# Performance work log

Measured on AMD Instinct MI355X. Metric: run time of the kernel, lower is better.

The kernel has to match this reference:

```python
import jax, jax.numpy as jnp
import numpy as np

B, NQ, NKV, D = 2, 2048, 4096, 1024
H, DH = 16, 64            # qk_channels = v_channels = 1024 -> 16 heads x 64
HID = 2 * int(4.0 * D)    # GEGLU produces 8192 -> split into 2x4096
EPS = 1e-6


def layernorm(x, scale, bias):
    mu = jnp.mean(x, axis=-1, keepdims=True)
    var = jnp.mean(jnp.square(x - mu), axis=-1, keepdims=True)
    return (x - mu) * jax.lax.rsqrt(var + EPS) * scale + bias


def setup_inputs() -> dict:
    key = jax.random.key(0)
    ks = jax.random.split(key, 12)
    s = 0.02
    return {
        "inputs_q": jax.random.normal(ks[0], (B, NQ, D), jnp.float32),
        "inputs_kv": jax.random.normal(ks[1], (B, NKV, D), jnp.float32),
        "ln_q_scale": jnp.ones((D,), jnp.float32),
        "ln_q_bias": jnp.zeros((D,), jnp.float32),
        "ln_kv_scale": jnp.ones((D,), jnp.float32),
        "ln_kv_bias": jnp.zeros((D,), jnp.float32),
        "Wq": s * jax.random.normal(ks[2], (D, H, DH), jnp.float32),
        "bq": jnp.zeros((H, DH), jnp.float32),
        "Wk": s * jax.random.normal(ks[3], (D, H, DH), jnp.float32),
        "bk": jnp.zeros((H, DH), jnp.float32),
        "Wv": s * jax.random.normal(ks[4], (D, H, DH), jnp.float32),
        "bv": jnp.zeros((H, DH), jnp.float32),
        "Wo": s * jax.random.normal(ks[5], (H, DH, D), jnp.float32),
        "bo": jnp.zeros((D,), jnp.float32),
        "ln2_scale": jnp.ones((D,), jnp.float32),
        "ln2_bias": jnp.zeros((D,), jnp.float32),
        "W1": s * jax.random.normal(ks[6], (D, HID), jnp.float32),
        "b1": jnp.zeros((HID,), jnp.float32),
        "W2": s * jax.random.normal(ks[7], (HID // 2, D), jnp.float32),
        "b2": jnp.zeros((D,), jnp.float32),
    }


def reference(inputs_q, inputs_kv, ln_q_scale, ln_q_bias, ln_kv_scale, ln_kv_bias,
              Wq, bq, Wk, bk, Wv, bv, Wo, bo, ln2_scale, ln2_bias, W1, b1, W2, b2):
    ln_q = layernorm(inputs_q, ln_q_scale, ln_q_bias)
    ln_kv = layernorm(inputs_kv, ln_kv_scale, ln_kv_bias)
    # multi-head projections: DenseGeneral to (H, DH)
    q = jnp.einsum('bqd,dhe->bqhe', ln_q, Wq) + bq
    k = jnp.einsum('bkd,dhe->bkhe', ln_kv, Wk) + bk
    v = jnp.einsum('bkd,dhe->bkhe', ln_kv, Wv) + bv
    # scaled dot-product attention (full score matrix, as in source)
    attn = jnp.einsum('bqhd,bkhd->bhqk', q, k) / np.sqrt(DH).astype(np.float32)
    attn = jax.nn.softmax(attn, axis=-1)
    o = jnp.einsum('bhqk,bkhd->bqhd', attn, v)
    # output projection contracting (H, DH)
    x = jnp.einsum('bqhd,hdo->bqo', o, Wo) + bo
    x = x + inputs_q  # query residual
    # GEGLU MLP
    h = layernorm(x, ln2_scale, ln2_bias)
    h = jnp.dot(h, W1) + b1
    a, g = jnp.split(h, 2, axis=-1)
    h = a * jax.nn.gelu(g)  # approximate (tanh) gelu, flax default
    y = jnp.dot(h, W2) + b2
    return x + y
```

## Files before the change

### kernel.cpp

```cpp
#include <hip/hip_runtime.h>

typedef unsigned short u16;
typedef unsigned int u32;
typedef float f32x4 __attribute__((ext_vector_type(4)));
typedef float f32x16 __attribute__((ext_vector_type(16)));
typedef __bf16 bf16x8 __attribute__((ext_vector_type(8)));
typedef short s16x8 __attribute__((ext_vector_type(8)));
typedef short s16x4 __attribute__((ext_vector_type(4)));
typedef u32 u32x4 __attribute__((ext_vector_type(4)));

#define MFMA16(a, b, c) __builtin_amdgcn_mfma_f32_16x16x32_bf16((a), (b), (c), 0, 0, 0)
#define MFMA32(a, b, c) __builtin_amdgcn_mfma_f32_32x32x16_bf16((a), (b), (c), 0, 0, 0)

typedef const __attribute__((address_space(1))) void* gas1_t;
typedef __attribute__((address_space(3))) void* las3_t;
#define GLDS16(g, l) __builtin_amdgcn_global_load_lds((gas1_t)(g), (las3_t)(l), 16, 0, 0)

static __device__ __forceinline__ u16 f2bf(float f) {
  u32 u = __builtin_bit_cast(u32, f);
  u += 0x7FFFu + ((u >> 16) & 1u);
  return (u16)(u >> 16);
}
static __device__ __forceinline__ u32 cvtpk(float lo, float hi) {
  u32 r;
  asm("v_cvt_pk_bf16_f32 %0, %1, %2" : "=v"(r) : "v"(lo), "v"(hi));
  return r;
}
static __device__ __forceinline__ float gelu_t(float g) {
  float u = 0.7978845608f * (g + 0.044715f * g * g * g);
  float e = __expf(2.0f * u);
  float t = 1.0f - 2.0f / (e + 1.0f);
  return 0.5f * g * (1.0f + t);
}

__global__ __launch_bounds__(256) void prep_weights(const float* __restrict__ Wq,
                                                    const float* __restrict__ Wk,
                                                    const float* __restrict__ Wv,
                                                    const float* __restrict__ Wo,
                                                    const float* __restrict__ W1,
                                                    const float* __restrict__ W2,
                                                    u16* __restrict__ wqt,
                                                    u16* __restrict__ wkvt,
                                                    u16* __restrict__ wot,
                                                    u16* __restrict__ w1i,
                                                    u16* __restrict__ w2t, float qsc) {
  __shared__ u16 t[64][72];
  const int id = blockIdx.x;
  const int tid = threadIdx.x;
  auto tileT = [&](const float* in, u16* out, int K, int N, int k0, int n0, float scale) {
#pragma unroll
    for (int i = 0; i < 16; ++i) {
      int idx = tid + i * 256;
      int r = idx >> 6, c = idx & 63;
      t[r][c] = f2bf(in[(size_t)(k0 + r) * N + n0 + c] * scale);
    }
    __syncthreads();
#pragma unroll
    for (int i = 0; i < 16; ++i) {
      int idx = tid + i * 256;
      int r = idx >> 6, c = idx & 63;
      out[(size_t)(n0 + r) * K + k0 + c] = t[c][r];
    }
  };
  if (id < 256) {
    tileT(Wq, wqt, 1024, 1024, (id & 15) * 64, (id >> 4) * 64, qsc);
  } else if (id < 512) {
    int i2 = id - 256;
    tileT(Wk, wkvt, 1024, 1024, (i2 & 15) * 64, (i2 >> 4) * 64, 1.0f);
  } else if (id < 768) {
    int i2 = id - 512;
    tileT(Wv, wkvt + 1024 * 1024, 1024, 1024, (i2 & 15) * 64, (i2 >> 4) * 64, 1.0f);
  } else if (id < 1024) {
    int i2 = id - 768;
    tileT(Wo, wot, 1024, 1024, (i2 & 15) * 64, (i2 >> 4) * 64, 1.0f);
  } else if (id < 3072) {
    int i2 = id - 1024;
    int k0 = (i2 & 15) * 64, n0 = (i2 >> 4) * 64;
#pragma unroll
    for (int i = 0; i < 16; ++i) {
      int idx = tid + i * 256;
      int r = idx >> 6, c = idx & 63;
      int np = n0 + c;
      int orig = ((np >> 5) << 4) + (np & 15) + (((np >> 4) & 1) << 12);
      t[r][c] = f2bf(W1[(size_t)(k0 + r) * 8192 + orig]);
    }
    __syncthreads();
#pragma unroll
    for (int i = 0; i < 16; ++i) {
      int idx = tid + i * 256;
      int r = idx >> 6, c = idx & 63;
      w1i[(size_t)(n0 + r) * 1024 + k0 + c] = t[c][r];
    }
  } else {
    int i3 = id - 3072;
    tileT(W2, w2t, 4096, 1024, (i3 & 63) * 64, (i3 >> 6) * 64, 1.0f);
  }
}

__global__ __launch_bounds__(256) void ln_fused(const float* __restrict__ xq,
                                                const float* __restrict__ xkv,
                                                const float* __restrict__ scq,
                                                const float* __restrict__ biq,
                                                const float* __restrict__ sckv,
                                                const float* __restrict__ bikv,
                                                u16* __restrict__ outq,
                                                u16* __restrict__ outkv) {
  const int id = blockIdx.x;
  const bool isq = id < 4096;
  const int row = isq ? id : id - 4096;
  const float* x = isq ? xq : xkv;
  const float* sc = isq ? scq : sckv;
  const float* bi = isq ? biq : bikv;
  u16* out = isq ? outq : outkv;
  int tid = threadIdx.x;
  float4 v = ((const float4*)(x + (size_t)row * 1024))[tid];
  float s = v.x + v.y + v.z + v.w;
  float s2 = v.x * v.x + v.y * v.y + v.z * v.z + v.w * v.w;
  for (int m = 1; m < 64; m <<= 1) {
    s += __shfl_xor(s, m);
    s2 += __shfl_xor(s2, m);
  }
  __shared__ float rs[4], rs2[4];
  int wave = tid >> 6, lane = tid & 63;
  if (lane == 0) { rs[wave] = s; rs2[wave] = s2; }
  __syncthreads();
  s = rs[0] + rs[1] + rs[2] + rs[3];
  s2 = rs2[0] + rs2[1] + rs2[2] + rs2[3];
  float mu = s * (1.0f / 1024.0f);
  float var = s2 * (1.0f / 1024.0f) - mu * mu;
  float inv = rsqrtf(var + 1e-6f);
  float4 scv = ((const float4*)sc)[tid];
  float4 biv = ((const float4*)bi)[tid];
  s16x4 o;
  o[0] = (short)f2bf((v.x - mu) * inv * scv.x + biv.x);
  o[1] = (short)f2bf((v.y - mu) * inv * scv.y + biv.y);
  o[2] = (short)f2bf((v.z - mu) * inv * scv.z + biv.z);
  o[3] = (short)f2bf((v.w - mu) * inv * scv.w + biv.w);
  *(s16x4*)(out + (size_t)row * 1024 + tid * 4) = o;
}

template <int MODE>
__global__ __launch_bounds__(256) void gemm_nt(const u16* __restrict__ A,
                                               const u16* __restrict__ Bt,
                                               const float* __restrict__ bias,
                                               const float* __restrict__ resid,
                                               void* __restrict__ Cout,
                                               int M, int N, int K, float bias_scale) {
  __shared__ u16 As[128 * 64];
  __shared__ u16 Bs[128 * 64];
  const int nbx = gridDim.x;
  const int nwg = nbx * gridDim.y;
  const int wg0 = blockIdx.y * nbx + blockIdx.x;
  const int wg = (nwg & 7) ? wg0 : (wg0 & 7) * (nwg >> 3) + (wg0 >> 3);
  const int m0 = (wg % nbx) * 128, n0 = (wg / nbx) * 128;
  const int tid = threadIdx.x;
  const int lane = tid & 63, wave = tid >> 6;
  const int wm = (wave >> 1) * 64, wn = (wave & 1) * 64;
  const int lr = lane & 15, hi4 = lane >> 4;
  f32x4 acc[4][4] = {};
  for (int k0 = 0; k0 < K; k0 += 64) {
#pragma unroll
    for (int i = 0; i < 4; ++i) {
      int s = i * 256 + tid;
      int r = s >> 3, slot = s & 7;
      int gslot = slot ^ (r & 7);
      int ldst = (i * 256 + wave * 64) * 8;
      GLDS16(A + (size_t)(m0 + r) * K + k0 + gslot * 8, &As[ldst]);
      GLDS16(Bt + (size_t)(n0 + r) * K + k0 + gslot * 8, &Bs[ldst]);
    }
    __syncthreads();
#pragma unroll
    for (int ks = 0; ks < 2; ++ks) {
      const int sl = ((ks * 4 + hi4) ^ (lr & 7)) * 8;
      bf16x8 af[4], bfr[4];
#pragma unroll
      for (int t = 0; t < 4; ++t) {
        af[t] = __builtin_bit_cast(bf16x8, *(const s16x8*)&As[(wm + t * 16 + lr) * 64 + sl]);
        bfr[t] = __builtin_bit_cast(bf16x8, *(const s16x8*)&Bs[(wn + t * 16 + lr) * 64 + sl]);
      }
#pragma unroll
      for (int mt = 0; mt < 4; ++mt)
#pragma unroll
        for (int nt = 0; nt < 4; ++nt)
          acc[mt][nt] = MFMA16(af[mt], bfr[nt], acc[mt][nt]);
    }
    __syncthreads();
  }
#pragma unroll
  for (int mt = 0; mt < 4; ++mt) {
#pragma unroll
    for (int nt = 0; nt < 4; ++nt) {
      const int ncol = n0 + wn + nt * 16 + lr;
      const float bv = bias[ncol] * bias_scale;
      const int mbase = m0 + wm + mt * 16 + hi4 * 4;
#pragma unroll
      for (int r = 0; r < 4; ++r) {
        const int m = mbase + r;
        const float val = acc[mt][nt][r] + bv;
        if constexpr (MODE == 0) {
          ((u16*)Cout)[(size_t)m * N + ncol] = f2bf(val);
        } else {
          ((float*)Cout)[(size_t)m * N + ncol] = val + resid[(size_t)m * N + ncol];
        }
      }
    }
  }
}

template <int MODE>
__global__ __launch_bounds__(512, 2) void gemm256(const u16* __restrict__ A,
                                                  const u16* __restrict__ Bt,
                                                  const float* __restrict__ bias,
                                                  const float* __restrict__ bias2,
                                                  u16* __restrict__ Cout,
                                                  u16* __restrict__ Vout,
                                                  int M, int N, int K, int nmajor) {
  __shared__ __align__(16) u16 sA[2][2][256 * 32];
  __shared__ __align__(16) u16 sB[2][2][256 * 32];
  const int nbx = M >> 8, nby = N >> 8;
  const int nblk = nbx * nby;
  const int cpx = nblk >> 3;
  const int wg0 = blockIdx.x;
  const int wg = (wg0 & 7) * cpx + (wg0 >> 3);
  int mi, ni;
  if (nmajor) { ni = wg % nby; mi = wg / nby; } else { mi = wg % nbx; ni = wg / nbx; }
  const int m0 = mi << 8, n0 = ni << 8;
  const int tid = threadIdx.x;
  const int lane = tid & 63, wave = tid >> 6;
  const int wr = wave >> 2, wc = wave & 3;
  const int lr = lane & 15, hi4 = lane >> 4;
  const int rdoct = (hi4 ^ ((lr >> 1) & 3)) * 8;
  const int NT = K >> 6;

  auto stageA = [&](int t, int kh) {
#pragma unroll
    for (int i = 0; i < 2; ++i) {
      int idx = i * 512 + tid;
      int r = idx >> 2, go = (idx & 3) ^ ((r >> 1) & 3);
      GLDS16(A + (size_t)(m0 + r) * K + t * 64 + kh * 32 + go * 8,
             &sA[t & 1][kh][(i * 512 + wave * 64) * 8]);
    }
  };
  auto stageB = [&](int t, int kh) {
#pragma unroll
    for (int i = 0; i < 2; ++i) {
      int idx = i * 512 + tid;
      int r = idx >> 2, go = (idx & 3) ^ ((r >> 1) & 3);
      GLDS16(Bt + (size_t)(n0 + r) * K + t * 64 + kh * 32 + go * 8,
             &sB[t & 1][kh][(i * 512 + wave * 64) * 8]);
    }
  };

  f32x4 acc[8][4] = {};
  bf16x8 af[4], bf[4];

  stageA(0, 0); stageB(0, 0); stageA(0, 1); stageB(0, 1);
  asm volatile("s_waitcnt vmcnt(4)" ::: "memory");
  __builtin_amdgcn_s_barrier();
  __builtin_amdgcn_sched_barrier(0);

  for (int t = 0; t < NT; ++t) {
    const int buf = t & 1;
    const bool pre = (t + 1 < NT);
#pragma unroll
    for (int kh = 0; kh < 2; ++kh) {
#pragma unroll
      for (int nt = 0; nt < 4; ++nt)
        bf[nt] = __builtin_bit_cast(bf16x8,
            *(const s16x8*)&sB[buf][kh][(wc * 64 + nt * 16 + lr) * 32 + rdoct]);
#pragma unroll
      for (int mf = 0; mf < 4; ++mf)
        af[mf] = __builtin_bit_cast(bf16x8,
            *(const s16x8*)&sA[buf][kh][(wr * 128 + mf * 16 + lr) * 32 + rdoct]);
      if (pre) stageA(t + 1, kh);
      __builtin_amdgcn_s_barrier();
      asm volatile("s_waitcnt lgkmcnt(0)" ::: "memory");
      __builtin_amdgcn_sched_barrier(0);
      __builtin_amdgcn_s_setprio(1);
#pragma unroll
      for (int mf = 0; mf < 4; ++mf)
#pragma unroll
        for (int nt = 0; nt < 4; ++nt)
          acc[mf][nt] = MFMA16(af[mf], bf[nt], acc[mf][nt]);
      __builtin_amdgcn_s_setprio(0);
      __builtin_amdgcn_s_barrier();
      __builtin_amdgcn_sched_barrier(0);
#pragma unroll
      for (int mf = 0; mf < 4; ++mf)
        af[mf] = __builtin_bit_cast(bf16x8,
            *(const s16x8*)&sA[buf][kh][(wr * 128 + (4 + mf) * 16 + lr) * 32 + rdoct]);
      if (pre) stageB(t + 1, kh);
      __builtin_amdgcn_s_barrier();
      asm volatile("s_waitcnt lgkmcnt(0)" ::: "memory");
      __builtin_amdgcn_sched_barrier(0);
      __builtin_amdgcn_s_setprio(1);
#pragma unroll
      for (int mf = 0; mf < 4; ++mf)
#pragma unroll
        for (int nt = 0; nt < 4; ++nt)
          acc[4 + mf][nt] = MFMA16(af[mf], bf[nt], acc[4 + mf][nt]);
      __builtin_amdgcn_s_setprio(0);
      if (pre)
        asm volatile("s_waitcnt vmcnt(4)" ::: "memory");
      else
        asm volatile("s_waitcnt vmcnt(0)" ::: "memory");
      __builtin_amdgcn_s_barrier();
      __builtin_amdgcn_sched_barrier(0);
    }
  }

  if constexpr (MODE == 0) {
#pragma unroll
    for (int mf = 0; mf < 8; ++mf) {
#pragma unroll
      for (int nt = 0; nt < 4; ++nt) {
        const int ncol = n0 + wc * 64 + nt * 16 + lr;
        const int mbase = m0 + wr * 128 + mf * 16 + hi4 * 4;
        const bool isk = ncol < 1024;
        const int vc = isk ? ncol : ncol - 1024;
        const float bv = isk ? bias[ncol] : bias2[vc];
#pragma unroll
        for (int r = 0; r < 4; ++r) {
          const int m = mbase + r;
          const float val = acc[mf][nt][r] + bv;
          if (isk) {
            Cout[(size_t)m * 1024 + ncol] = f2bf(val);
          } else {
            size_t vidx = ((size_t)((m >> 12) * 1024 + vc) << 12) | (size_t)(m & 4095);
            Vout[vidx] = f2bf(val);
          }
        }
      }
    }
  } else {
#pragma unroll
    for (int mf = 0; mf < 8; ++mf) {
      const int mbase = m0 + wr * 128 + mf * 16 + hi4 * 4;
#pragma unroll
      for (int p = 0; p < 2; ++p) {
        const int oc = (((n0 + wc * 64 + p * 32) >> 5) << 4) + lr;
        const float ba = bias[oc];
        const float bg = bias[oc + 4096];
#pragma unroll
        for (int r = 0; r < 4; ++r) {
          const int m = mbase + r;
          float a = acc[mf][2 * p][r] + ba;
          float g = acc[mf][2 * p + 1][r] + bg;
          Cout[(size_t)m * 4096 + oc] = f2bf(a * gelu_t(g));
        }
      }
    }
  }
}

__global__ __launch_bounds__(256, 2) void flash_attn(const u16* __restrict__ Qg,
                                                     const u16* __restrict__ Kg,
                                                     const u16* __restrict__ Vt,
                                                     u16* __restrict__ Og) {
  __shared__ u16 Ks[2][64 * 64];
  __shared__ u16 Vs[2][64 * 64];
  const int id = blockIdx.x;
  const int bh = (id & 7) * 4 + ((id >> 3) & 3);
  const int qb = id >> 5;
  const int b = bh >> 4, h = bh & 15;
  const int q0 = qb * 128;
  const int tid = threadIdx.x;
  const int lane = tid & 63, wave = tid >> 6;
  const int lq = lane & 31, hi = lane >> 5;
  const u16* Kbase = Kg + (size_t)(b * 4096) * 1024 + h * 64;
  const u16* Vbase = Vt + (size_t)((b * 16 + h) * 64) * 4096;
  bf16x8 qf[4];
  const size_t qrow = (size_t)(b * 2048 + q0 + wave * 32 + lq);
#pragma unroll
  for (int dc = 0; dc < 4; ++dc)
    qf[dc] = __builtin_bit_cast(bf16x8, *(const s16x8*)&Qg[qrow * 1024 + h * 64 + dc * 16 + hi * 8]);

  f32x16 oacc0 = {}, oacc1 = {};
  float lrun = 0.0f;

  auto stage = [&](int buf, int tile) {
    const int kv0 = tile * 64;
#pragma unroll
    for (int i = 0; i < 2; ++i) {
      int s = i * 256 + tid;
      int r = s >> 3;
      int inb = ((s & 7) * 16) ^ ((r & 7) << 4);
      GLDS16(Kbase + (size_t)(kv0 + r) * 1024 + (inb >> 1), &Ks[buf][(i * 256 + wave * 64) * 8]);
    }
#pragma unroll
    for (int i = 0; i < 2; ++i) {
      int s = i * 256 + tid;
      int r = s >> 3;
      int inb = ((s & 7) * 16) ^ ((r & 7) << 4);
      GLDS16(Vbase + (size_t)r * 4096 + kv0 + (inb >> 1), &Vs[buf][(i * 256 + wave * 64) * 8]);
    }
  };

  stage(0, 0);
  __syncthreads();
  int cur = 0;
  for (int t = 0; t < 64; ++t) {
    if (t < 63) stage(cur ^ 1, t + 1);
    f32x16 sA = {}, sB = {};
    __builtin_amdgcn_s_setprio(1);
#pragma unroll
    for (int dc = 0; dc < 4; ++dc) {
      int row = lq;
      int inb = (dc * 32 + hi * 16) ^ ((row & 7) << 4);
      bf16x8 kf = __builtin_bit_cast(bf16x8, *(const s16x8*)&Ks[cur][row * 64 + (inb >> 1)]);
      sA = MFMA32(kf, qf[dc], sA);
    }
#pragma unroll
    for (int dc = 0; dc < 4; ++dc) {
      int row = 32 + lq;
      int inb = (dc * 32 + hi * 16) ^ ((row & 7) << 4);
      bf16x8 kf = __builtin_bit_cast(bf16x8, *(const s16x8*)&Ks[cur][row * 64 + (inb >> 1)]);
      sB = MFMA32(kf, qf[dc], sB);
    }
    __builtin_amdgcn_s_setprio(0);
    float ts = 0.0f;
#pragma unroll
    for (int i = 0; i < 16; ++i) {
      float p = __builtin_amdgcn_exp2f(sA[i]);
      sA[i] = p;
      ts += p;
    }
#pragma unroll
    for (int i = 0; i < 16; ++i) {
      float p = __builtin_amdgcn_exp2f(sB[i]);
      sB[i] = p;
      ts += p;
    }
    ts += __shfl_xor(ts, 32);
    lrun += ts;
    u32 wa[8], wb[8];
#pragma unroll
    for (int i = 0; i < 8; ++i) wa[i] = cvtpk(sA[2 * i], sA[2 * i + 1]);
#pragma unroll
    for (int i = 0; i < 8; ++i) wb[i] = cvtpk(sB[2 * i], sB[2 * i + 1]);
    u32 a0 = wa[0], c0 = wa[2];
    asm("v_permlane32_swap_b32 %0, %1" : "+v"(a0), "+v"(c0));
    u32 a1 = wa[1], c1 = wa[3];
    asm("v_permlane32_swap_b32 %0, %1" : "+v"(a1), "+v"(c1));
    u32 a2 = wa[4], c2 = wa[6];
    asm("v_permlane32_swap_b32 %0, %1" : "+v"(a2), "+v"(c2));
    u32 a3 = wa[5], c3 = wa[7];
    asm("v_permlane32_swap_b32 %0, %1" : "+v"(a3), "+v"(c3));
    u32 e0 = wb[0], g0 = wb[2];
    asm("v_permlane32_swap_b32 %0, %1" : "+v"(e0), "+v"(g0));
    u32 e1 = wb[1], g1 = wb[3];
    asm("v_permlane32_swap_b32 %0, %1" : "+v"(e1), "+v"(g1));
    u32 e2 = wb[4], g2 = wb[6];
    asm("v_permlane32_swap_b32 %0, %1" : "+v"(e2), "+v"(g2));
    u32 e3 = wb[5], g3 = wb[7];
    asm("v_permlane32_swap_b32 %0, %1" : "+v"(e3), "+v"(g3));
    u32x4 t00 = {a0, a1, c0, c1};
    u32x4 t01 = {a2, a3, c2, c3};
    u32x4 t10 = {e0, e1, g0, g1};
    u32x4 t11 = {e2, e3, g2, g3};
    bf16x8 p00 = __builtin_bit_cast(bf16x8, t00);
    bf16x8 p01 = __builtin_bit_cast(bf16x8, t01);
    bf16x8 p10 = __builtin_bit_cast(bf16x8, t10);
    bf16x8 p11 = __builtin_bit_cast(bf16x8, t11);
    __builtin_amdgcn_s_setprio(1);
#pragma unroll
    for (int st = 0; st < 2; ++st) {
      bf16x8 pc0 = st ? p10 : p00;
      bf16x8 pc1 = st ? p11 : p01;
#pragma unroll
      for (int c = 0; c < 2; ++c) {
        bf16x8 pf = c ? pc1 : pc0;
        {
          int row = lq;
          int inb = (st * 64 + c * 32 + hi * 16) ^ ((row & 7) << 4);
          bf16x8 vf = __builtin_bit_cast(bf16x8, *(const s16x8*)&Vs[cur][row * 64 + (inb >> 1)]);
          oacc0 = MFMA32(vf, pf, oacc0);
        }
        {
          int row = 32 + lq;
          int inb = (st * 64 + c * 32 + hi * 16) ^ ((row & 7) << 4);
          bf16x8 vf = __builtin_bit_cast(bf16x8, *(const s16x8*)&Vs[cur][row * 64 + (inb >> 1)]);
          oacc1 = MFMA32(vf, pf, oacc1);
        }
      }
    }
    __builtin_amdgcn_s_setprio(0);
    __syncthreads();
    cur ^= 1;
  }
  float rinv = 1.0f / lrun;
  u16* obase = Og + qrow * 1024 + h * 64;
#pragma unroll
  for (int rp = 0; rp < 8; ++rp) {
    int r0 = rp * 2;
    int d0 = (r0 & 3) + 8 * (r0 >> 2) + 4 * hi;
    *(u32*)&obase[d0] = cvtpk(oacc0[r0] * rinv, oacc0[r0 + 1] * rinv);
    *(u32*)&obase[32 + d0] = cvtpk(oacc1[r0] * rinv, oacc1[r0 + 1] * rinv);
  }
}

extern "C" void kernel_launch(void* const* d_in, const int* in_sizes, int n_in,
                              void* d_out, int out_size, void* d_ws, size_t ws_size,
                              hipStream_t stream) {
  (void)in_sizes; (void)n_in; (void)out_size; (void)ws_size;
  const float* inputs_q = (const float*)d_in[0];
  const float* inputs_kv = (const float*)d_in[1];
  const float* ln_q_scale = (const float*)d_in[2];
  const float* ln_q_bias = (const float*)d_in[3];
  const float* ln_kv_scale = (const float*)d_in[4];
  const float* ln_kv_bias = (const float*)d_in[5];
  const float* Wq = (const float*)d_in[6];
  const float* bq = (const float*)d_in[7];
  const float* Wk = (const float*)d_in[8];
  const float* bk = (const float*)d_in[9];
  const float* Wv = (const float*)d_in[10];
  const float* bv = (const float*)d_in[11];
  const float* Wo = (const float*)d_in[12];
  const float* bo = (const float*)d_in[13];
  const float* ln2_scale = (const float*)d_in[14];
  const float* ln2_bias = (const float*)d_in[15];
  const float* W1 = (const float*)d_in[16];
  const float* b1 = (const float*)d_in[17];
  const float* W2 = (const float*)d_in[18];
  const float* b2 = (const float*)d_in[19];
  float* out = (float*)d_out;
  char* ws = (char*)d_ws;
  const size_t MB = 1ull << 20;
  u16* lnq = (u16*)(ws + 0);
  u16* lnkv = (u16*)(ws + 8 * MB);
  u16* Qb = (u16*)(ws + 24 * MB);
  u16* Kb = (u16*)(ws + 32 * MB);
  u16* Vtb = (u16*)(ws + 48 * MB);
  u16* Ob = (u16*)(ws + 64 * MB);
  float* xbuf = (float*)(ws + 72 * MB);
  u16* ln2b = (u16*)(ws + 88 * MB);
  u16* gg = (u16*)(ws + 96 * MB);
  u16* wqt = (u16*)(ws + 128 * MB);
  u16* wkvt = (u16*)(ws + 130 * MB);
  u16* wot = (u16*)(ws + 134 * MB);
  u16* w1i = (u16*)(ws + 136 * MB);
  u16* w2t = (u16*)(ws + 152 * MB);

  const float QSC = 0.125f * 1.44269504088896f;
  dim3 blk(256);
  prep_weights<<<dim3(4096), blk, 0, stream>>>(Wq, Wk, Wv, Wo, W1, W2, wqt, wkvt, wot, w1i, w2t, QSC);
  ln_fused<<<dim3(12288), blk, 0, stream>>>(inputs_q, inputs_kv, ln_q_scale, ln_q_bias,
                                            ln_kv_scale, ln_kv_bias, lnq, lnkv);
  gemm_nt<0><<<dim3(32, 8), blk, 0, stream>>>(lnq, wqt, bq, nullptr, Qb, 4096, 1024, 1024, QSC);
  gemm256<0><<<dim3(256), dim3(512), 0, stream>>>(lnkv, wkvt, bk, bv, Kb, Vtb, 8192, 2048, 1024, 1);
  flash_attn<<<dim3(512), blk, 0, stream>>>(Qb, Kb, Vtb, Ob);
  gemm_nt<2><<<dim3(32, 8), blk, 0, stream>>>(Ob, wot, bo, inputs_q, xbuf, 4096, 1024, 1024, 1.0f);
  ln_fused<<<dim3(4096), blk, 0, stream>>>(xbuf, xbuf, ln2_scale, ln2_bias, ln2_scale, ln2_bias,
                                           ln2b, ln2b);
  gemm256<1><<<dim3(512), dim3(512), 0, stream>>>(ln2b, w1i, b1, nullptr, gg, nullptr, 4096, 8192, 1024, 0);
  gemm_nt<2><<<dim3(32, 8), blk, 0, stream>>>(gg, w2t, b2, xbuf, out, 4096, 1024, 4096, 1.0f);
}
```

Measured before the change: 388.4 us.

## Merge prep and LN kernels, double-buffer gemm_nt, compute softmax sum via MFMA

```diff
diff --git a/kernel.cpp b/kernel.cpp
--- a/kernel.cpp
+++ b/kernel.cpp
@@ -33,20 +33,62 @@
   return 0.5f * g * (1.0f + t);
 }
 
-__global__ __launch_bounds__(256) void prep_weights(const float* __restrict__ Wq,
-                                                    const float* __restrict__ Wk,
-                                                    const float* __restrict__ Wv,
-                                                    const float* __restrict__ Wo,
-                                                    const float* __restrict__ W1,
-                                                    const float* __restrict__ W2,
-                                                    u16* __restrict__ wqt,
-                                                    u16* __restrict__ wkvt,
-                                                    u16* __restrict__ wot,
-                                                    u16* __restrict__ w1i,
-                                                    u16* __restrict__ w2t, float qsc) {
+__global__ __launch_bounds__(256) void prep_all(const float* __restrict__ Wq,
+                                                const float* __restrict__ Wk,
+                                                const float* __restrict__ Wv,
+                                                const float* __restrict__ Wo,
+                                                const float* __restrict__ W1,
+                                                const float* __restrict__ W2,
+                                                u16* __restrict__ wqt,
+                                                u16* __restrict__ wkvt,
+                                                u16* __restrict__ wot,
+                                                u16* __restrict__ w1i,
+                                                u16* __restrict__ w2t, float qsc,
+                                                const float* __restrict__ xq,
+                                                const float* __restrict__ xkv,
+                                                const float* __restrict__ scq,
+                                                const float* __restrict__ biq,
+                                                const float* __restrict__ sckv,
+                                                const float* __restrict__ bikv,
+                                                u16* __restrict__ outq,
+                                                u16* __restrict__ outkv) {
   __shared__ u16 t[64][72];
+  __shared__ float rs[4], rs2[4];
   const int id = blockIdx.x;
   const int tid = threadIdx.x;
+  if (id >= 4096) {
+    const int rid = id - 4096;
+    const bool isq = rid < 4096;
+    const int row = isq ? rid : rid - 4096;
+    const float* x = isq ? xq : xkv;
+    const float* sc = isq ? scq : sckv;
+    const float* bi = isq ? biq : bikv;
+    u16* out = isq ? outq : outkv;
+    float4 v = ((const float4*)(x + (size_t)row * 1024))[tid];
+    float s = v.x + v.y + v.z + v.w;
+    float s2 = v.x * v.x + v.y * v.y + v.z * v.z + v.w * v.w;
+    for (int m = 1; m < 64; m <<= 1) {
+      s += __shfl_xor(s, m);
+      s2 += __shfl_xor(s2, m);
+    }
+    int wave = tid >> 6, lane = tid & 63;
+    if (lane == 0) { rs[wave] = s; rs2[wave] = s2; }
+    __syncthreads();
+    s = rs[0] + rs[1] + rs[2] + rs[3];
+    s2 = rs2[0] + rs2[1] + rs2[2] + rs2[3];
+    float mu = s * (1.0f / 1024.0f);
+    float var = s2 * (1.0f / 1024.0f) - mu * mu;
+    float inv = rsqrtf(var + 1e-6f);
+    float4 scv = ((const float4*)sc)[tid];
+    float4 biv = ((const float4*)bi)[tid];
+    s16x4 o;
+    o[0] = (short)f2bf((v.x - mu) * inv * scv.x + biv.x);
+    o[1] = (short)f2bf((v.y - mu) * inv * scv.y + biv.y);
+    o[2] = (short)f2bf((v.z - mu) * inv * scv.z + biv.z);
+    o[3] = (short)f2bf((v.w - mu) * inv * scv.w + biv.w);
+    *(s16x4*)(out + (size_t)row * 1024 + tid * 4) = o;
+    return;
+  }
   auto tileT = [&](const float* in, u16* out, int K, int N, int k0, int n0, float scale) {
 #pragma unroll
     for (int i = 0; i < 16; ++i) {
@@ -98,22 +140,12 @@
 }
 
 __global__ __launch_bounds__(256) void ln_fused(const float* __restrict__ xq,
-                                                const float* __restrict__ xkv,
-                                                const float* __restrict__ scq,
-                                                const float* __restrict__ biq,
-                                                const float* __restrict__ sckv,
-                                                const float* __restrict__ bikv,
-                                                u16* __restrict__ outq,
-                                                u16* __restrict__ outkv) {
-  const int id = blockIdx.x;
-  const bool isq = id < 4096;
-  const int row = isq ? id : id - 4096;
-  const float* x = isq ? xq : xkv;
-  const float* sc = isq ? scq : sckv;
-  const float* bi = isq ? biq : bikv;
-  u16* out = isq ? outq : outkv;
+                                                const float* __restrict__ sc,
+                                                const float* __restrict__ bi,
+                                                u16* __restrict__ out) {
+  const int row = blockIdx.x;
   int tid = threadIdx.x;
-  float4 v = ((const float4*)(x + (size_t)row * 1024))[tid];
+  float4 v = ((const float4*)(xq + (size_t)row * 1024))[tid];
   float s = v.x + v.y + v.z + v.w;
   float s2 = v.x * v.x + v.y * v.y + v.z * v.z + v.w * v.w;
   for (int m = 1; m < 64; m <<= 1) {
@@ -146,8 +178,8 @@
                                                const float* __restrict__ resid,
                                                void* __restrict__ Cout,
                                                int M, int N, int K, float bias_scale) {
-  __shared__ u16 As[128 * 64];
-  __shared__ u16 Bs[128 * 64];
+  __shared__ u16 As[2][128 * 64];
+  __shared__ u16 Bs[2][128 * 64];
   const int nbx = gridDim.x;
   const int nwg = nbx * gridDim.y;
   const int wg0 = blockIdx.y * nbx + blockIdx.x;
@@ -157,34 +189,45 @@
   const int lane = tid & 63, wave = tid >> 6;
   const int wm = (wave >> 1) * 64, wn = (wave & 1) * 64;
   const int lr = lane & 15, hi4 = lane >> 4;
-  f32x4 acc[4][4] = {};
-  for (int k0 = 0; k0 < K; k0 += 64) {
+  const int NT = K >> 6;
+  auto stage = [&](int t, int buf) {
 #pragma unroll
     for (int i = 0; i < 4; ++i) {
       int s = i * 256 + tid;
       int r = s >> 3, slot = s & 7;
       int gslot = slot ^ (r & 7);
       int ldst = (i * 256 + wave * 64) * 8;
-      GLDS16(A + (size_t)(m0 + r) * K + k0 + gslot * 8, &As[ldst]);
-      GLDS16(Bt + (size_t)(n0 + r) * K + k0 + gslot * 8, &Bs[ldst]);
-    }
-    __syncthreads();
+      GLDS16(A + (size_t)(m0 + r) * K + t * 64 + gslot * 8, &As[buf][ldst]);
+      GLDS16(Bt + (size_t)(n0 + r) * K + t * 64 + gslot * 8, &Bs[buf][ldst]);
+    }
+  };
+  f32x4 acc[4][4] = {};
+  stage(0, 0);
+  asm volatile("s_waitcnt vmcnt(0)" ::: "memory");
+  __builtin_amdgcn_s_barrier();
+  int buf = 0;
+  for (int t = 0; t < NT; ++t) {
+    if (t + 1 < NT) stage(t + 1, buf ^ 1);
 #pragma unroll
     for (int ks = 0; ks < 2; ++ks) {
       const int sl = ((ks * 4 + hi4) ^ (lr & 7)) * 8;
       bf16x8 af[4], bfr[4];
 #pragma unroll
-      for (int t = 0; t < 4; ++t) {
-        af[t] = __builtin_bit_cast(bf16x8, *(const s16x8*)&As[(wm + t * 16 + lr) * 64 + sl]);
-        bfr[t] = __builtin_bit_cast(bf16x8, *(const s16x8*)&Bs[(wn + t * 16 + lr) * 64 + sl]);
+      for (int tt = 0; tt < 4; ++tt) {
+        af[tt] = __builtin_bit_cast(bf16x8, *(const s16x8*)&As[buf][(wm + tt * 16 + lr) * 64 + sl]);
+        bfr[tt] = __builtin_bit_cast(bf16x8, *(const s16x8*)&Bs[buf][(wn + tt * 16 + lr) * 64 + sl]);
       }
+      __builtin_amdgcn_s_setprio(1);
 #pragma unroll
       for (int mt = 0; mt < 4; ++mt)
 #pragma unroll
         for (int nt = 0; nt < 4; ++nt)
           acc[mt][nt] = MFMA16(af[mt], bfr[nt], acc[mt][nt]);
-    }
-    __syncthreads();
+      __builtin_amdgcn_s_setprio(0);
+    }
+    asm volatile("s_waitcnt vmcnt(0) lgkmcnt(0)" ::: "memory");
+    __builtin_amdgcn_s_barrier();
+    buf ^= 1;
   }
 #pragma unroll
   for (int mt = 0; mt < 4; ++mt) {
@@ -375,8 +418,9 @@
   for (int dc = 0; dc < 4; ++dc)
     qf[dc] = __builtin_bit_cast(bf16x8, *(const s16x8*)&Qg[qrow * 1024 + h * 64 + dc * 16 + hi * 8]);
 
-  f32x16 oacc0 = {}, oacc1 = {};
-  float lrun = 0.0f;
+  const u32x4 onesw = {0x3F803F80u, 0x3F803F80u, 0x3F803F80u, 0x3F803F80u};
+  const bf16x8 ones = __builtin_bit_cast(bf16x8, onesw);
+  f32x16 oacc0 = {}, oacc1 = {}, accl = {};
 
   auto stage = [&](int buf, int tile) {
     const int kv0 = tile * 64;
@@ -396,43 +440,28 @@
     }
   };
 
-  stage(0, 0);
-  __syncthreads();
-  int cur = 0;
-  for (int t = 0; t < 64; ++t) {
-    if (t < 63) stage(cur ^ 1, t + 1);
+  auto computeT = [&](const u16* __restrict__ Kbuf, const u16* __restrict__ Vbuf) {
     f32x16 sA = {}, sB = {};
     __builtin_amdgcn_s_setprio(1);
 #pragma unroll
     for (int dc = 0; dc < 4; ++dc) {
       int row = lq;
       int inb = (dc * 32 + hi * 16) ^ ((row & 7) << 4);
-      bf16x8 kf = __builtin_bit_cast(bf16x8, *(const s16x8*)&Ks[cur][row * 64 + (inb >> 1)]);
+      bf16x8 kf = __builtin_bit_cast(bf16x8, *(const s16x8*)&Kbuf[row * 64 + (inb >> 1)]);
       sA = MFMA32(kf, qf[dc], sA);
     }
 #pragma unroll
     for (int dc = 0; dc < 4; ++dc) {
       int row = 32 + lq;
       int inb = (dc * 32 + hi * 16) ^ ((row & 7) << 4);
-      bf16x8 kf = __builtin_bit_cast(bf16x8, *(const s16x8*)&Ks[cur][row * 64 + (inb >> 1)]);
+      bf16x8 kf = __builtin_bit_cast(bf16x8, *(const s16x8*)&Kbuf[row * 64 + (inb >> 1)]);
       sB = MFMA32(kf, qf[dc], sB);
     }
     __builtin_amdgcn_s_setprio(0);
-    float ts = 0.0f;
-#pragma unroll
-    for (int i = 0; i < 16; ++i) {
-      float p = __builtin_amdgcn_exp2f(sA[i]);
-      sA[i] = p;
-      ts += p;
-    }
-#pragma unroll
-    for (int i = 0; i < 16; ++i) {
-      float p = __builtin_amdgcn_exp2f(sB[i]);
-      sB[i] = p;
-      ts += p;
-    }
-    ts += __shfl_xor(ts, 32);
-    lrun += ts;
+#pragma unroll
+    for (int i = 0; i < 16; ++i) sA[i] = __builtin_amdgcn_exp2f(sA[i]);
+#pragma unroll
+    for (int i = 0; i < 16; ++i) sB[i] = __builtin_amdgcn_exp2f(sB[i]);
     u32 wa[8], wb[8];
 #pragma unroll
     for (int i = 0; i < 8; ++i) wa[i] = cvtpk(sA[2 * i], sA[2 * i + 1]);
@@ -458,37 +487,42 @@
     u32x4 t01 = {a2, a3, c2, c3};
     u32x4 t10 = {e0, e1, g0, g1};
     u32x4 t11 = {e2, e3, g2, g3};
-    bf16x8 p00 = __builtin_bit_cast(bf16x8, t00);
-    bf16x8 p01 = __builtin_bit_cast(bf16x8, t01);
-    bf16x8 p10 = __builtin_bit_cast(bf16x8, t10);
-    bf16x8 p11 = __builtin_bit_cast(bf16x8, t11);
+    bf16x8 pf[4] = {__builtin_bit_cast(bf16x8, t00), __builtin_bit_cast(bf16x8, t01),
+                    __builtin_bit_cast(bf16x8, t10), __builtin_bit_cast(bf16x8, t11)};
     __builtin_amdgcn_s_setprio(1);
 #pragma unroll
-    for (int st = 0; st < 2; ++st) {
-      bf16x8 pc0 = st ? p10 : p00;
-      bf16x8 pc1 = st ? p11 : p01;
+    for (int st = 0; st < 2; ++st)
 #pragma unroll
       for (int c = 0; c < 2; ++c) {
-        bf16x8 pf = c ? pc1 : pc0;
+        const int pi = st * 2 + c;
         {
           int row = lq;
           int inb = (st * 64 + c * 32 + hi * 16) ^ ((row & 7) << 4);
-          bf16x8 vf = __builtin_bit_cast(bf16x8, *(const s16x8*)&Vs[cur][row * 64 + (inb >> 1)]);
-          oacc0 = MFMA32(vf, pf, oacc0);
+          bf16x8 vf = __builtin_bit_cast(bf16x8, *(const s16x8*)&Vbuf[row * 64 + (inb >> 1)]);
+          oacc0 = MFMA32(vf, pf[pi], oacc0);
         }
         {
           int row = 32 + lq;
           int inb = (st * 64 + c * 32 + hi * 16) ^ ((row & 7) << 4);
-          bf16x8 vf = __builtin_bit_cast(bf16x8, *(const s16x8*)&Vs[cur][row * 64 + (inb >> 1)]);
-          oacc1 = MFMA32(vf, pf, oacc1);
+          bf16x8 vf = __builtin_bit_cast(bf16x8, *(const s16x8*)&Vbuf[row * 64 + (inb >> 1)]);
+          oacc1 = MFMA32(vf, pf[pi], oacc1);
         }
+        accl = MFMA32(ones, pf[pi], accl);
       }
-    }
     __builtin_amdgcn_s_setprio(0);
+  };
+
+  stage(0, 0);
+  __syncthreads();
+  for (int t = 0; t < 64; t += 2) {
+    if (t + 1 < 64) stage(1, t + 1);
+    computeT(Ks[0], Vs[0]);
     __syncthreads();
-    cur ^= 1;
-  }
-  float rinv = 1.0f / lrun;
+    if (t + 2 < 64) stage(0, t + 2);
+    computeT(Ks[1], Vs[1]);
+    __syncthreads();
+  }
+  float rinv = 1.0f / accl[0];
   u16* obase = Og + qrow * 1024 + h * 64;
 #pragma unroll
   for (int rp = 0; rp < 8; ++rp) {
@@ -543,15 +577,14 @@
 
   const float QSC = 0.125f * 1.44269504088896f;
   dim3 blk(256);
-  prep_weights<<<dim3(4096), blk, 0, stream>>>(Wq, Wk, Wv, Wo, W1, W2, wqt, wkvt, wot, w1i, w2t, QSC);
-  ln_fused<<<dim3(12288), blk, 0, stream>>>(inputs_q, inputs_kv, ln_q_scale, ln_q_bias,
+  prep_all<<<dim3(16384), blk, 0, stream>>>(Wq, Wk, Wv, Wo, W1, W2, wqt, wkvt, wot, w1i, w2t, QSC,
+                                            inputs_q, inputs_kv, ln_q_scale, ln_q_bias,
                                             ln_kv_scale, ln_kv_bias, lnq, lnkv);
   gemm_nt<0><<<dim3(32, 8), blk, 0, stream>>>(lnq, wqt, bq, nullptr, Qb, 4096, 1024, 1024, QSC);
   gemm256<0><<<dim3(256), dim3(512), 0, stream>>>(lnkv, wkvt, bk, bv, Kb, Vtb, 8192, 2048, 1024, 1);
   flash_attn<<<dim3(512), blk, 0, stream>>>(Qb, Kb, Vtb, Ob);
   gemm_nt<2><<<dim3(32, 8), blk, 0, stream>>>(Ob, wot, bo, inputs_q, xbuf, 4096, 1024, 1024, 1.0f);
-  ln_fused<<<dim3(4096), blk, 0, stream>>>(xbuf, xbuf, ln2_scale, ln2_bias, ln2_scale, ln2_bias,
-                                           ln2b, ln2b);
+  ln_fused<<<dim3(4096), blk, 0, stream>>>(xbuf, ln2_scale, ln2_bias, ln2b);
   gemm256<1><<<dim3(512), dim3(512), 0, stream>>>(ln2b, w1i, b1, nullptr, gg, nullptr, 4096, 8192, 1024, 0);
   gemm_nt<2><<<dim3(32, 8), blk, 0, stream>>>(gg, w2t, b2, xbuf, out, 4096, 1024, 4096, 1.0f);
 }
```

New measurement: 376.7 us. 3.0% less time.
